# Kernel optimization log

Measured on AMD Instinct MI355X. Metric: run time of the kernel, lower is better.

## Reference

```python
import jax, jax.numpy as jnp
import numpy as np

B, N, D, P = 4, 4096, 64, 2
M, H = 64, 128
ARENA = 20.0  # positions uniform in [0, ARENA]^2; radius 1.0 -> ~32 neighbors


def _mlp2(x, Wa, ba, Wb, bb):
    return jax.nn.relu(x @ Wa + ba) @ Wb + bb


def setup_inputs() -> dict:
    key = jax.random.key(0)
    ks = jax.random.split(key, 14)
    def lin(k, fan_in, fan_out):
        bound = 1.0 / np.sqrt(fan_in)
        kw, kb = jax.random.split(k)
        W = jax.random.uniform(kw, (fan_in, fan_out), jnp.float32, -bound, bound)
        b = jax.random.uniform(kb, (fan_out,), jnp.float32, -bound, bound)
        return W, b
    W1, b1 = lin(ks[0], D, H)
    W2, b2 = lin(ks[1], H, M)
    W3, b3 = lin(ks[2], 2 * M, H)
    W4, b4 = lin(ks[3], H, M)
    W5, b5 = lin(ks[4], D + M, H)
    W6, b6 = lin(ks[5], H, D)
    agent_states = jax.random.normal(ks[6], (B, N, D), jnp.float32)
    agent_positions = jax.random.uniform(ks[7], (B, N, P), jnp.float32) * ARENA
    return {
        "agent_states": agent_states,
        "agent_positions": agent_positions,
        "neighbor_radius": 1,
        "W1": W1, "b1": b1, "W2": W2, "b2": b2,
        "W3": W3, "b3": b3, "W4": W4, "b4": b4,
        "W5": W5, "b5": b5, "W6": W6, "b6": b6,
    }


def reference(agent_states, agent_positions, neighbor_radius,
              W1, b1, W2, b2, W3, b3, W4, b4, W5, b5, W6, b6):
    n = agent_states.shape[1]
    # message encoder MLP: [B,N,D] -> [B,N,M]
    messages = _mlp2(agent_states, W1, b1, W2, b2)
    # dense pairwise distances [B,N,N] (faithful to original O(N^2) mask)
    diff = agent_positions[:, :, None, :] - agent_positions[:, None, :, :]
    distances = jnp.sqrt(jnp.sum(diff * diff, axis=-1))
    adj = (distances < jnp.float32(neighbor_radius)).astype(messages.dtype)
    adj = adj * (1.0 - jnp.eye(n, dtype=messages.dtype))[None]
    deg = jnp.clip(jnp.sum(adj, axis=-1, keepdims=True), 1.0, None)
    adj = adj / deg
    # vectorized form of the per-agent gather-aggregate loop
    aggregated = jnp.einsum('bij,bjm->bim', adj, messages)
    combined = jnp.concatenate([messages, aggregated], axis=-1)
    final_msgs = _mlp2(combined, W3, b3, W4, b4)
    feats = jnp.concatenate([agent_states, final_msgs], axis=-1)
    out = _mlp2(feats, W5, b5, W6, b6)
    return agent_states + out
```

## Files before the change

### kernel.cpp

```cpp
#include <hip/hip_runtime.h>

typedef unsigned short u16;
typedef unsigned int u32;
typedef __bf16 bf16x8 __attribute__((ext_vector_type(8)));
typedef unsigned short ushort8 __attribute__((ext_vector_type(8)));
typedef float f32x4 __attribute__((ext_vector_type(4)));

#define DEV_INLINE __device__ __forceinline__

constexpr int NB = 4;
constexpr int NAG = 4096;
constexpr int ROWS = NB * NAG;
constexpr int GRID = 20;
constexpr int CELLS = GRID * GRID;
constexpr int CSTRIDE = 404;
constexpr int MAXNB = 128;

DEV_INLINE u16 f2bu(float x) { __bf16 h = (__bf16)x; return __builtin_bit_cast(u16, h); }
DEV_INLINE float bu2f(u16 u) { return __builtin_bit_cast(float, ((u32)u) << 16); }
DEV_INLINE u32 pack2(float a, float b) { return (u32)f2bu(a) | ((u32)f2bu(b) << 16); }

DEV_INLINE f32x4 MF(bf16x8 a, const u16* p, f32x4 c) {
  ushort8 bu = *(const ushort8*)p;
  return __builtin_amdgcn_mfma_f32_16x16x32_bf16(a, __builtin_bit_cast(bf16x8, bu), c, 0, 0, 0);
}

template<bool BF>
DEV_INLINE bf16x8 loadA(const void* __restrict__ src, int row, int c) {
  if constexpr (BF) {
    ushort8 u = *reinterpret_cast<const ushort8*>((const u16*)src + (size_t)row * 64 + c);
    return __builtin_bit_cast(bf16x8, u);
  } else {
    const float* f = (const float*)src + (size_t)row * 64 + c;
    f32x4 a = *(const f32x4*)f;
    f32x4 b = *(const f32x4*)(f + 4);
    bf16x8 r;
    r[0] = (__bf16)a[0]; r[1] = (__bf16)a[1]; r[2] = (__bf16)a[2]; r[3] = (__bf16)a[3];
    r[4] = (__bf16)b[0]; r[5] = (__bf16)b[1]; r[6] = (__bf16)b[2]; r[7] = (__bf16)b[3];
    return r;
  }
}

__global__ __launch_bounds__(1024) void fused_setup_mlp1(
    const float* __restrict__ pos, const float* __restrict__ states,
    const float* __restrict__ W1, const float* __restrict__ b1,
    const float* __restrict__ W2, const float* __restrict__ b2,
    const float* __restrict__ W3, const float* __restrict__ W4,
    const float* __restrict__ W5, const float* __restrict__ W6,
    u16* __restrict__ wts, u16* __restrict__ msgs,
    float2* __restrict__ pos_sorted, int* __restrict__ cell_start,
    int* __restrict__ sid)
{
  extern __shared__ u16 smem[];
  const int tid = threadIdx.x;
  const int lane = tid & 63;
  const int wave = tid >> 6;
  const int bid = blockIdx.x;

  if (bid < NB) {
    int* cnt_s = (int*)smem;
    int* start_s = cnt_s + CELLS;
    u16* cell_of = (u16*)(start_s + CELLS + 1);
    u16* rank_of = cell_of + NAG;
    const float2* pb = (const float2*)(pos + (size_t)bid * NAG * 2);
    for (int c = tid; c < CELLS; c += 1024) cnt_s[c] = 0;
    __syncthreads();
    for (int i = tid; i < NAG; i += 1024) {
      float2 p = pb[i];
      int cx = min(max((int)floorf(p.x), 0), GRID - 1);
      int cy = min(max((int)floorf(p.y), 0), GRID - 1);
      int c = cy * GRID + cx;
      rank_of[i] = (u16)atomicAdd(&cnt_s[c], 1);
      cell_of[i] = (u16)c;
    }
    __syncthreads();
    if (wave == 0) {
      int carry = 0;
      for (int g = 0; g < CELLS; g += 64) {
        int c = g + lane;
        int x = (c < CELLS) ? cnt_s[c] : 0;
#pragma unroll
        for (int off = 1; off < 64; off <<= 1) {
          int y = __shfl_up(x, off, 64);
          if (lane >= off) x += y;
        }
        if (c < CELLS) start_s[c + 1] = carry + x;
        carry += __shfl(x, 63, 64);
      }
      if (lane == 0) start_s[0] = 0;
    }
    __syncthreads();
    for (int c = tid; c <= CELLS; c += 1024) cell_start[bid * CSTRIDE + c] = start_s[c];
    for (int i = tid; i < NAG; i += 1024) {
      int kk = start_s[cell_of[i]] + (int)rank_of[i];
      sid[bid * NAG + kk] = bid * NAG + i;
      pos_sorted[bid * NAG + kk] = pb[i];
    }
    return;
  }

  if (bid >= NB + 256) {
    const int base = (bid - (NB + 256)) * 12288;
#pragma unroll
    for (int t = 0; t < 12; ++t) {
      int idx = base + t * 1024 + tid;
      const float* src; int n, k, Nc;
      if (idx < 16384)      { src = W3; n = idx >> 7; k = idx & 127; Nc = 128; }
      else if (idx < 24576) { int li = idx - 16384; src = W4; n = li >> 7; k = li & 127; Nc = 64; }
      else if (idx < 40960) { int li = idx - 24576; src = W5; n = li >> 7; k = li & 127; Nc = 128; }
      else                  { int li = idx - 40960; src = W6; n = li >> 7; k = li & 127; Nc = 64; }
      wts[idx] = f2bu(src[k * Nc + n]);
    }
    return;
  }

  u16* WaTs = smem;
  u16* WbTs = smem + 9216;
  u16* ovl  = smem + 17920;

  const int l15 = lane & 15;
  const int khalf = (lane >> 4) * 8;
  const int rg = wave >> 2;
  const int cq = wave & 3;
  const int rb = (bid - NB) * 64 + rg * 16;
  const int row = rb + l15;

  bf16x8 aS[2];
  aS[0] = loadA<false>(states, row, khalf);
  aS[1] = loadA<false>(states, row, 32 + khalf);

  for (int t = tid; t < 4096; t += 1024) {
    const int e = t * 2;
    const int k = e >> 7, n = e & 127;
    const float2 v = *(const float2*)&W1[e];
    *(u32*)&ovl[k * 132 + n] = pack2(v.x, v.y);
  }
  __syncthreads();
  {
    const int n = tid & 127, g = tid >> 7;
    ushort8 v;
#pragma unroll
    for (int j = 0; j < 8; ++j) v[j] = ovl[(g * 8 + j) * 132 + n];
    *(ushort8*)&WaTs[n * 72 + g * 8] = v;
  }
  __syncthreads();
  for (int t = tid; t < 4096; t += 1024) {
    const int e = t * 2;
    const int k = e >> 6, n = e & 63;
    const float2 v = *(const float2*)&W2[e];
    *(u32*)&ovl[k * 68 + n] = pack2(v.x, v.y);
  }
  __syncthreads();
  {
    const int n = tid & 63, g = tid >> 6;
    ushort8 v;
#pragma unroll
    for (int j = 0; j < 8; ++j) v[j] = ovl[(g * 8 + j) * 68 + n];
    *(ushort8*)&WbTs[n * 136 + g * 8] = v;
  }
  __syncthreads();

  u16* hs = ovl + rg * 2176;

  f32x4 acc1[2] = {};
#pragma unroll
  for (int kt = 0; kt < 2; ++kt) {
#pragma unroll
    for (int j = 0; j < 2; ++j) {
      const int nt = cq * 2 + j;
      acc1[j] = MF(aS[kt], &WaTs[(nt * 16 + l15) * 72 + kt * 32 + khalf], acc1[j]);
    }
  }
#pragma unroll
  for (int j = 0; j < 2; ++j) {
    const int col = (cq * 2 + j) * 16 + l15;
    const float bv = b1[col];
#pragma unroll
    for (int r = 0; r < 4; ++r)
      hs[((lane >> 4) * 4 + r) * 136 + col] = f2bu(fmaxf(acc1[j][r] + bv, 0.0f));
  }
  __syncthreads();

  f32x4 acc2 = {};
#pragma unroll
  for (int kt = 0; kt < 4; ++kt) {
    ushort8 au = *(const ushort8*)&hs[l15 * 136 + kt * 32 + khalf];
    acc2 = MF(__builtin_bit_cast(bf16x8, au),
              &WbTs[(cq * 16 + l15) * 136 + kt * 32 + khalf], acc2);
  }
  {
    const int col = cq * 16 + l15;
    const float bv = b2[col];
#pragma unroll
    for (int r = 0; r < 4; ++r)
      msgs[(size_t)(rb + (lane >> 4) * 4 + r) * 64 + col] = f2bu(acc2[r] + bv);
  }
}

__global__ __launch_bounds__(256) void agg_kernel(
    const float2* __restrict__ pos_sorted, const u16* __restrict__ msgs,
    const int* __restrict__ cell_start, const int* __restrict__ sid,
    const int* __restrict__ radius_ptr, u16* __restrict__ aggr)
{
  __shared__ u16 idxb[4][MAXNB];
  const int b = blockIdx.y;
  const int lane = threadIdx.x & 63;
  const int wave = threadIdx.x >> 6;
  const int k = blockIdx.x * 4 + wave;
  const float2* pb = pos_sorted + (size_t)b * NAG;
  const float2 pk = pb[k];
  const float r = (float)(*radius_ptr);
  const float r2 = __fmul_rn(r, r);
  const int cx = min(max((int)floorf(pk.x), 0), GRID - 1);
  const int cy = min(max((int)floorf(pk.y), 0), GRID - 1);
  const int* cs = cell_start + b * CSTRIDE;
  const int* sb = sid + b * NAG;
  const unsigned long long lt = (1ull << lane) - 1ull;

  int cnt = 0;
#pragma unroll
  for (int dy = -1; dy <= 1; ++dy) {
    const int yy = cy + dy;
    if (yy < 0 || yy >= GRID) continue;
    const int x0 = max(cx - 1, 0), x1 = min(cx + 1, GRID - 1);
    const int c0 = cs[yy * GRID + x0];
    const int c1 = cs[yy * GRID + x1 + 1];
    for (int base = c0; base < c1; base += 64) {
      const int j = base + lane;
      bool ok = false;
      if (j < c1) {
        const float2 pj = pb[j];
        const float dx_ = pk.x - pj.x;
        const float dy_ = pk.y - pj.y;
        const float d2 = __fadd_rn(__fmul_rn(dx_, dx_), __fmul_rn(dy_, dy_));
        ok = (d2 < r2) && (j != k);
      }
      const unsigned long long m = __ballot(ok);
      if (ok) {
        const int p = cnt + __popcll(m & lt);
        if (p < MAXNB) idxb[wave][p] = (u16)sb[j];
      }
      cnt += (int)__popcll(m);
    }
  }

  const int q = lane & 15;
  const int s = lane >> 4;
  const int n = min(cnt, MAXNB);
  float a0 = 0.0f, a1 = 0.0f, a2 = 0.0f, a3 = 0.0f;
  const int nfull = n & ~3;
  for (int g = 0; g < nfull; g += 4) {
    const int jj = (int)idxb[wave][g + s];
    const uint2 v = *(const uint2*)(msgs + (size_t)jj * 64 + q * 4);
    a0 += __builtin_bit_cast(float, v.x << 16);
    a1 += __builtin_bit_cast(float, v.x & 0xffff0000u);
    a2 += __builtin_bit_cast(float, v.y << 16);
    a3 += __builtin_bit_cast(float, v.y & 0xffff0000u);
  }
  const int t = n - nfull;
  if (s < t) {
    const int jj = (int)idxb[wave][nfull + s];
    const uint2 v = *(const uint2*)(msgs + (size_t)jj * 64 + q * 4);
    a0 += __builtin_bit_cast(float, v.x << 16);
    a1 += __builtin_bit_cast(float, v.x & 0xffff0000u);
    a2 += __builtin_bit_cast(float, v.y << 16);
    a3 += __builtin_bit_cast(float, v.y & 0xffff0000u);
  }
  a0 += __shfl_xor(a0, 16); a1 += __shfl_xor(a1, 16);
  a2 += __shfl_xor(a2, 16); a3 += __shfl_xor(a3, 16);
  a0 += __shfl_xor(a0, 32); a1 += __shfl_xor(a1, 32);
  a2 += __shfl_xor(a2, 32); a3 += __shfl_xor(a3, 32);

  if (s == 0) {
    const float inv = 1.0f / (float)(cnt > 0 ? cnt : 1);
    const int orow = sb[k];
    uint2 w;
    w.x = pack2(a0 * inv, a1 * inv);
    w.y = pack2(a2 * inv, a3 * inv);
    *(uint2*)(aggr + (size_t)orow * 64 + q * 4) = w;
  }
}

__global__ __launch_bounds__(1024, 4) void mlp23_kernel(
    const float* __restrict__ states, const u16* __restrict__ msgs,
    const u16* __restrict__ aggr, const u16* __restrict__ wts,
    const float* __restrict__ b3, const float* __restrict__ b4,
    const float* __restrict__ b5, const float* __restrict__ b6,
    float* __restrict__ out)
{
  extern __shared__ u16 smem[];
  u16* W3s = smem;
  u16* W4s = W3s + 128 * 136;
  u16* W5s = W4s + 64 * 136;
  u16* W6s = W5s + 128 * 136;
  u16* hsb = W6s + 64 * 136;
  u16* fsb = hsb + 4 * 16 * 136;

  const int tid = threadIdx.x;
  const int lane = tid & 63;
  const int wave = tid >> 6;
  const int rg = wave >> 2;
  const int cq = wave & 3;
  const int l15 = lane & 15;
  const int khalf = (lane >> 4) * 8;
  const int rb = blockIdx.x * 64 + rg * 16;
  const int row = rb + l15;
  u16* hs = hsb + rg * (16 * 136);
  u16* fs = fsb + rg * (16 * 136);

  bf16x8 aM[2], aG[2], aS[2];
  aM[0] = loadA<true>(msgs, row, khalf);
  aM[1] = loadA<true>(msgs, row, 32 + khalf);
  aG[0] = loadA<true>(aggr, row, khalf);
  aG[1] = loadA<true>(aggr, row, 32 + khalf);
  aS[0] = loadA<false>(states, row, khalf);
  aS[1] = loadA<false>(states, row, 32 + khalf);

  for (int t = tid; t < 6144; t += 1024) {
    const int e = t * 8;
    ushort8 v = *(const ushort8*)&wts[e];
    u16* dst;
    if (e < 16384)      dst = &W3s[(e >> 7) * 136 + (e & 127)];
    else if (e < 24576) { int li = e - 16384; dst = &W4s[(li >> 7) * 136 + (li & 127)]; }
    else if (e < 40960) { int li = e - 24576; dst = &W5s[(li >> 7) * 136 + (li & 127)]; }
    else                { int li = e - 40960; dst = &W6s[(li >> 7) * 136 + (li & 127)]; }
    *(ushort8*)dst = v;
  }
  __syncthreads();

  f32x4 acc1[2] = {};
#pragma unroll
  for (int kt = 0; kt < 4; ++kt) {
    bf16x8 a = (kt < 2) ? aM[kt] : aG[kt - 2];
#pragma unroll
    for (int j = 0; j < 2; ++j) {
      const int nt = cq * 2 + j;
      acc1[j] = MF(a, &W3s[(nt * 16 + l15) * 136 + kt * 32 + khalf], acc1[j]);
    }
  }
#pragma unroll
  for (int j = 0; j < 2; ++j) {
    const int col = (cq * 2 + j) * 16 + l15;
    const float bv = b3[col];
#pragma unroll
    for (int r = 0; r < 4; ++r)
      hs[((lane >> 4) * 4 + r) * 136 + col] = f2bu(fmaxf(acc1[j][r] + bv, 0.0f));
  }
  __syncthreads();

  f32x4 acc2 = {};
#pragma unroll
  for (int kt = 0; kt < 4; ++kt) {
    ushort8 au = *(const ushort8*)&hs[l15 * 136 + kt * 32 + khalf];
    acc2 = MF(__builtin_bit_cast(bf16x8, au),
              &W4s[(cq * 16 + l15) * 136 + kt * 32 + khalf], acc2);
  }
  {
    const int col = cq * 16 + l15;
    const float bv = b4[col];
#pragma unroll
    for (int r = 0; r < 4; ++r)
      fs[((lane >> 4) * 4 + r) * 136 + col] = f2bu(acc2[r] + bv);
  }
  __syncthreads();

  f32x4 acc3[2] = {};
#pragma unroll
  for (int kt = 0; kt < 4; ++kt) {
    bf16x8 a;
    if (kt < 2) a = aS[kt];
    else {
      ushort8 au = *(const ushort8*)&fs[l15 * 136 + (kt - 2) * 32 + khalf];
      a = __builtin_bit_cast(bf16x8, au);
    }
#pragma unroll
    for (int j = 0; j < 2; ++j) {
      const int nt = cq * 2 + j;
      acc3[j] = MF(a, &W5s[(nt * 16 + l15) * 136 + kt * 32 + khalf], acc3[j]);
    }
  }
#pragma unroll
  for (int j = 0; j < 2; ++j) {
    const int col = (cq * 2 + j) * 16 + l15;
    const float bv = b5[col];
#pragma unroll
    for (int r = 0; r < 4; ++r)
      hs[((lane >> 4) * 4 + r) * 136 + col] = f2bu(fmaxf(acc3[j][r] + bv, 0.0f));
  }
  __syncthreads();

  f32x4 acc4 = {};
#pragma unroll
  for (int kt = 0; kt < 4; ++kt) {
    ushort8 au = *(const ushort8*)&hs[l15 * 136 + kt * 32 + khalf];
    acc4 = MF(__builtin_bit_cast(bf16x8, au),
              &W6s[(cq * 16 + l15) * 136 + kt * 32 + khalf], acc4);
  }
  {
    const int col = cq * 16 + l15;
    const float bv = b6[col];
#pragma unroll
    for (int r = 0; r < 4; ++r) {
      const int m = (lane >> 4) * 4 + r;
      const size_t o = (size_t)(rb + m) * 64 + col;
      out[o] = acc4[r] + bv + states[o];
    }
  }
}

extern "C" void kernel_launch(void* const* d_in, const int* in_sizes, int n_in,
                              void* d_out, int out_size, void* d_ws, size_t ws_size,
                              hipStream_t stream) {
  const float* states = (const float*)d_in[0];
  const float* pos    = (const float*)d_in[1];
  const int*   radius = (const int*)d_in[2];
  const float* W1 = (const float*)d_in[3];
  const float* b1 = (const float*)d_in[4];
  const float* W2 = (const float*)d_in[5];
  const float* b2 = (const float*)d_in[6];
  const float* W3 = (const float*)d_in[7];
  const float* b3 = (const float*)d_in[8];
  const float* W4 = (const float*)d_in[9];
  const float* b4 = (const float*)d_in[10];
  const float* W5 = (const float*)d_in[11];
  const float* b5 = (const float*)d_in[12];
  const float* W6 = (const float*)d_in[13];
  const float* b6 = (const float*)d_in[14];
  float* out = (float*)d_out;

  u16* ws16 = (u16*)d_ws;
  u16* msgs = ws16;
  u16* aggr = msgs + (size_t)ROWS * 64;
  u16* wts  = aggr + (size_t)ROWS * 64;
  char* pbyte = (char*)(wts + 49152);
  float2* pos_sorted = (float2*)pbyte;
  int* cell_start = (int*)(pbyte + (size_t)ROWS * 8);
  int* sid = cell_start + NB * CSTRIDE;

  constexpr int LDS_K1 = 26624 * 2;
  constexpr int LDS_K3 = (384 * 136 + 8 * 16 * 136) * 2;

  fused_setup_mlp1<<<NB + 256 + 4, 1024, LDS_K1, stream>>>(
      pos, states, W1, b1, W2, b2, W3, W4, W5, W6,
      wts, msgs, pos_sorted, cell_start, sid);

  agg_kernel<<<dim3(NAG / 4, NB), 256, 0, stream>>>(
      pos_sorted, msgs, cell_start, sid, radius, aggr);

  mlp23_kernel<<<ROWS / 64, 1024, LDS_K3, stream>>>(
      states, msgs, aggr, wts, b3, b4, b5, b6, out);
}
```

Before: 41.88 us.

## Process four cell-sorted agents per wave sharing one candidate scan

Each wave in the aggregation kernel now handles four consecutive sorted agents. It scans the union of their neighbouring cells once, loading each candidate position and sorted id a single time and testing it against all four agents. This amortises global loads and loop overhead across agents. In exchange the grid has a quarter as many blocks, so parallelism drops, and the union region can hold more candidates than a single agent's 3x3 cells when the four agents sit in different cells.

```diff
diff --git a/kernel.cpp b/kernel.cpp
--- a/kernel.cpp
+++ b/kernel.cpp
@@ -202,82 +202,93 @@
     const int* __restrict__ cell_start, const int* __restrict__ sid,
     const int* __restrict__ radius_ptr, u16* __restrict__ aggr)
 {
-  __shared__ u16 idxb[4][MAXNB];
+  __shared__ u16 idxb[4][4][MAXNB];
   const int b = blockIdx.y;
   const int lane = threadIdx.x & 63;
   const int wave = threadIdx.x >> 6;
-  const int k = blockIdx.x * 4 + wave;
+  const int k0 = (blockIdx.x * 4 + wave) * 4;
   const float2* pb = pos_sorted + (size_t)b * NAG;
-  const float2 pk = pb[k];
   const float r = (float)(*radius_ptr);
   const float r2 = __fmul_rn(r, r);
-  const int cx = min(max((int)floorf(pk.x), 0), GRID - 1);
-  const int cy = min(max((int)floorf(pk.y), 0), GRID - 1);
   const int* cs = cell_start + b * CSTRIDE;
   const int* sb = sid + b * NAG;
   const unsigned long long lt = (1ull << lane) - 1ull;
 
-  int cnt = 0;
-#pragma unroll
-  for (int dy = -1; dy <= 1; ++dy) {
-    const int yy = cy + dy;
-    if (yy < 0 || yy >= GRID) continue;
-    const int x0 = max(cx - 1, 0), x1 = min(cx + 1, GRID - 1);
+  float2 pk[4];
+  int cnt[4] = {0, 0, 0, 0};
+  int cxmin = GRID, cxmax = -1, cymin = GRID, cymax = -1;
+#pragma unroll
+  for (int a = 0; a < 4; ++a) {
+    pk[a] = pb[k0 + a];
+    const int cx = min(max((int)floorf(pk[a].x), 0), GRID - 1);
+    const int cy = min(max((int)floorf(pk[a].y), 0), GRID - 1);
+    cxmin = min(cxmin, cx); cxmax = max(cxmax, cx);
+    cymin = min(cymin, cy); cymax = max(cymax, cy);
+  }
+  const int y0 = max(cymin - 1, 0), y1 = min(cymax + 1, GRID - 1);
+  const int x0 = max(cxmin - 1, 0), x1 = min(cxmax + 1, GRID - 1);
+
+  for (int yy = y0; yy <= y1; ++yy) {
     const int c0 = cs[yy * GRID + x0];
     const int c1 = cs[yy * GRID + x1 + 1];
     for (int base = c0; base < c1; base += 64) {
       const int j = base + lane;
-      bool ok = false;
-      if (j < c1) {
-        const float2 pj = pb[j];
-        const float dx_ = pk.x - pj.x;
-        const float dy_ = pk.y - pj.y;
+      const bool inb = j < c1;
+      float2 pj; pj.x = 1e30f; pj.y = 1e30f;
+      int sbj = 0;
+      if (inb) { pj = pb[j]; sbj = sb[j]; }
+#pragma unroll
+      for (int a = 0; a < 4; ++a) {
+        const float dx_ = pk[a].x - pj.x;
+        const float dy_ = pk[a].y - pj.y;
         const float d2 = __fadd_rn(__fmul_rn(dx_, dx_), __fmul_rn(dy_, dy_));
-        ok = (d2 < r2) && (j != k);
+        const bool ok = inb && (d2 < r2) && (j != k0 + a);
+        const unsigned long long m = __ballot(ok);
+        if (ok) {
+          const int p = cnt[a] + __popcll(m & lt);
+          if (p < MAXNB) idxb[wave][a][p] = (u16)sbj;
+        }
+        cnt[a] += (int)__popcll(m);
       }
-      const unsigned long long m = __ballot(ok);
-      if (ok) {
-        const int p = cnt + __popcll(m & lt);
-        if (p < MAXNB) idxb[wave][p] = (u16)sb[j];
-      }
-      cnt += (int)__popcll(m);
     }
   }
 
   const int q = lane & 15;
   const int s = lane >> 4;
-  const int n = min(cnt, MAXNB);
-  float a0 = 0.0f, a1 = 0.0f, a2 = 0.0f, a3 = 0.0f;
-  const int nfull = n & ~3;
-  for (int g = 0; g < nfull; g += 4) {
-    const int jj = (int)idxb[wave][g + s];
-    const uint2 v = *(const uint2*)(msgs + (size_t)jj * 64 + q * 4);
-    a0 += __builtin_bit_cast(float, v.x << 16);
-    a1 += __builtin_bit_cast(float, v.x & 0xffff0000u);
-    a2 += __builtin_bit_cast(float, v.y << 16);
-    a3 += __builtin_bit_cast(float, v.y & 0xffff0000u);
-  }
-  const int t = n - nfull;
-  if (s < t) {
-    const int jj = (int)idxb[wave][nfull + s];
-    const uint2 v = *(const uint2*)(msgs + (size_t)jj * 64 + q * 4);
-    a0 += __builtin_bit_cast(float, v.x << 16);
-    a1 += __builtin_bit_cast(float, v.x & 0xffff0000u);
-    a2 += __builtin_bit_cast(float, v.y << 16);
-    a3 += __builtin_bit_cast(float, v.y & 0xffff0000u);
-  }
-  a0 += __shfl_xor(a0, 16); a1 += __shfl_xor(a1, 16);
-  a2 += __shfl_xor(a2, 16); a3 += __shfl_xor(a3, 16);
-  a0 += __shfl_xor(a0, 32); a1 += __shfl_xor(a1, 32);
-  a2 += __shfl_xor(a2, 32); a3 += __shfl_xor(a3, 32);
-
-  if (s == 0) {
-    const float inv = 1.0f / (float)(cnt > 0 ? cnt : 1);
-    const int orow = sb[k];
-    uint2 w;
-    w.x = pack2(a0 * inv, a1 * inv);
-    w.y = pack2(a2 * inv, a3 * inv);
-    *(uint2*)(aggr + (size_t)orow * 64 + q * 4) = w;
+  for (int a = 0; a < 4; ++a) {
+    const int n = min(cnt[a], MAXNB);
+    float a0 = 0.0f, a1 = 0.0f, a2 = 0.0f, a3 = 0.0f;
+    const int nfull = n & ~3;
+    for (int g = 0; g < nfull; g += 4) {
+      const int jj = (int)idxb[wave][a][g + s];
+      const uint2 v = *(const uint2*)(msgs + (size_t)jj * 64 + q * 4);
+      a0 += __builtin_bit_cast(float, v.x << 16);
+      a1 += __builtin_bit_cast(float, v.x & 0xffff0000u);
+      a2 += __builtin_bit_cast(float, v.y << 16);
+      a3 += __builtin_bit_cast(float, v.y & 0xffff0000u);
+    }
+    const int t = n - nfull;
+    if (s < t) {
+      const int jj = (int)idxb[wave][a][nfull + s];
+      const uint2 v = *(const uint2*)(msgs + (size_t)jj * 64 + q * 4);
+      a0 += __builtin_bit_cast(float, v.x << 16);
+      a1 += __builtin_bit_cast(float, v.x & 0xffff0000u);
+      a2 += __builtin_bit_cast(float, v.y << 16);
+      a3 += __builtin_bit_cast(float, v.y & 0xffff0000u);
+    }
+    a0 += __shfl_xor(a0, 16); a1 += __shfl_xor(a1, 16);
+    a2 += __shfl_xor(a2, 16); a3 += __shfl_xor(a3, 16);
+    a0 += __shfl_xor(a0, 32); a1 += __shfl_xor(a1, 32);
+    a2 += __shfl_xor(a2, 32); a3 += __shfl_xor(a3, 32);
+
+    if (s == 0) {
+      const float inv = 1.0f / (float)(cnt[a] > 0 ? cnt[a] : 1);
+      const int orow = sb[k0 + a];
+      uint2 w;
+      w.x = pack2(a0 * inv, a1 * inv);
+      w.y = pack2(a2 * inv, a3 * inv);
+      *(uint2*)(aggr + (size_t)orow * 64 + q * 4) = w;
+    }
   }
 }
 
@@ -444,7 +455,7 @@
       pos, states, W1, b1, W2, b2, W3, W4, W5, W6,
       wts, msgs, pos_sorted, cell_start, sid);
 
-  agg_kernel<<<dim3(NAG / 4, NB), 256, 0, stream>>>(
+  agg_kernel<<<dim3(NAG / 16, NB), 256, 0, stream>>>(
       pos_sorted, msgs, cell_start, sid, radius, aggr);
 
   mlp23_kernel<<<ROWS / 64, 1024, LDS_K3, stream>>>(
```

Measured after the change: 45.40 us. 1.08x slower.
